# Kernel tuning notes

Hardware: AMD Instinct MI355X
Metric: run time of the kernel (lower is better)

Reference implementation:

```python
import jax, jax.numpy as jnp
import numpy as np


def setup_inputs() -> dict:
    key = jax.random.key(0)
    k1, k2 = jax.random.split(key)
    B, C, H, W = 8, 19, 512, 512
    pred = jax.random.normal(k1, (B, C, H, W), dtype=jnp.float32)
    target = jax.random.randint(k2, (B, H, W), 0, C, dtype=jnp.int64)
    return {"pred": pred, "target": target}


def reference(pred, target):
    # pred: (B, C, H, W) logits; target: (B, H, W) int labels. ignore_index=None.
    C = pred.shape[1]
    probs = jax.nn.softmax(pred, axis=1)
    # flatten pixels: (N, C)
    p = probs.transpose(0, 2, 3, 1).reshape(-1, C)
    t = target.reshape(-1)
    onehot = (t[:, None] == jnp.arange(C)[None, :]).astype(p.dtype)  # (N, C)
    errors = jnp.abs(onehot - p)                                     # (N, C)
    # descending sort of errors per class (batched over the class axis)
    order = jnp.argsort(-errors, axis=0)                             # (N, C)
    errors_sorted = jnp.take_along_axis(errors, order, axis=0)
    target_sorted = jnp.take_along_axis(onehot, order, axis=0)
    gts = target_sorted.sum(axis=0)                                  # (C,)
    intersection = gts[None, :] - jnp.cumsum(target_sorted, axis=0)
    union = gts[None, :] + jnp.cumsum(1.0 - target_sorted, axis=0)
    jaccard = 1.0 - intersection / union                             # (N, C)
    # Lovasz gradient: first-difference along sorted axis, keep first element
    grad = jnp.concatenate([jaccard[:1], jaccard[1:] - jaccard[:-1]], axis=0)
    per_class = jnp.sum(grad * errors_sorted, axis=0)                # (C,)
    present = gts > 0                                                # classes with pixels
    n_present = jnp.maximum(present.sum(), 1).astype(per_class.dtype)
    return jnp.where(present, per_class, 0.0).sum() / n_present
```

## Files before the change

### kernel.cpp

```cpp
#include <hip/hip_runtime.h>
#include <hip/hip_bf16.h>


#define NCLS 19
#define NB 512
#define HWSZ 262144
#define NPIX 2097152
#define HISTW (NCLS * NB)
#define RED_SPLIT 32
#define NBLK 512

__global__ __launch_bounds__(256) void lovasz_hist_kernel(
    const float* __restrict__ pred, const int* __restrict__ tgt,
    unsigned int* __restrict__ gh)
{
    __shared__ unsigned int lh[HISTW];
    for (int j = threadIdx.x; j < HISTW; j += 256) lh[j] = 0u;
    __syncthreads();

    const int stride = gridDim.x * 256;
    for (int g = blockIdx.x * 256 + threadIdx.x; g < (NPIX >> 2); g += stride) {
        const int idx = g << 2;
        const int b  = idx >> 18;
        const int hw = idx & (HWSZ - 1);
        const float* base = pred + ((size_t)b * NCLS) * HWSZ + hw;

        float x0[NCLS], x1[NCLS], x2[NCLS], x3[NCLS];
        #pragma unroll
        for (int c = 0; c < NCLS; ++c) {
            const float4 v = *(const float4*)(base + (size_t)c * HWSZ);
            x0[c] = v.x; x1[c] = v.y; x2[c] = v.z; x3[c] = v.w;
        }
        const int4 t4 = *(const int4*)(tgt + idx);

        float mx0 = x0[0], mx1 = x1[0], mx2 = x2[0], mx3 = x3[0];
        #pragma unroll
        for (int c = 1; c < NCLS; ++c) {
            mx0 = fmaxf(mx0, x0[c]); mx1 = fmaxf(mx1, x1[c]);
            mx2 = fmaxf(mx2, x2[c]); mx3 = fmaxf(mx3, x3[c]);
        }

        float s0 = 0.f, s1 = 0.f, s2 = 0.f, s3 = 0.f;
        #pragma unroll
        for (int c = 0; c < NCLS; ++c) {
            x0[c] = __expf(x0[c] - mx0); s0 += x0[c];
            x1[c] = __expf(x1[c] - mx1); s1 += x1[c];
            x2[c] = __expf(x2[c] - mx2); s2 += x2[c];
            x3[c] = __expf(x3[c] - mx3); s3 += x3[c];
        }
        const float inv0 = 1.f / s0, inv1 = 1.f / s1;
        const float inv2 = 1.f / s2, inv3 = 1.f / s3;

        #pragma unroll
        for (int c = 0; c < NCLS; ++c) {
            {
                const float p = x0[c] * inv0;
                const bool ist = (c == t4.x);
                const float e = ist ? (1.f - p) : p;
                int q = (int)(e * (float)NB);
                q = q < 0 ? 0 : (q > NB - 1 ? NB - 1 : q);
                atomicAdd(&lh[c * NB + q], ist ? 0x10001u : 1u);
            }
            {
                const float p = x1[c] * inv1;
                const bool ist = (c == t4.y);
                const float e = ist ? (1.f - p) : p;
                int q = (int)(e * (float)NB);
                q = q < 0 ? 0 : (q > NB - 1 ? NB - 1 : q);
                atomicAdd(&lh[c * NB + q], ist ? 0x10001u : 1u);
            }
            {
                const float p = x2[c] * inv2;
                const bool ist = (c == t4.z);
                const float e = ist ? (1.f - p) : p;
                int q = (int)(e * (float)NB);
                q = q < 0 ? 0 : (q > NB - 1 ? NB - 1 : q);
                atomicAdd(&lh[c * NB + q], ist ? 0x10001u : 1u);
            }
            {
                const float p = x3[c] * inv3;
                const bool ist = (c == t4.w);
                const float e = ist ? (1.f - p) : p;
                int q = (int)(e * (float)NB);
                q = q < 0 ? 0 : (q > NB - 1 ? NB - 1 : q);
                atomicAdd(&lh[c * NB + q], ist ? 0x10001u : 1u);
            }
        }
    }
    __syncthreads();

    unsigned int* dst = gh + (size_t)blockIdx.x * HISTW;
    for (int j = threadIdx.x; j < HISTW; j += 256) dst[j] = lh[j];
}

__global__ __launch_bounds__(256) void lovasz_reduce_kernel(
    const unsigned int* __restrict__ gh,
    unsigned int* __restrict__ cntp, unsigned int* __restrict__ tcntp, int nblk)
{
    const int j = blockIdx.x * 256 + threadIdx.x;
    const int k = blockIdx.y;
    const int nper = (nblk + RED_SPLIT - 1) / RED_SPLIT;
    const int b0 = k * nper;
    int b1 = b0 + nper; if (b1 > nblk) b1 = nblk;

    unsigned int cs = 0, ts = 0;
    for (int b = b0; b < b1; ++b) {
        const unsigned int w = gh[(size_t)b * HISTW + j];
        cs += w & 0xFFFFu;
        ts += w >> 16;
    }
    cntp[(size_t)k * HISTW + j] = cs;
    tcntp[(size_t)k * HISTW + j] = ts;
}

__global__ __launch_bounds__(512) void lovasz_perclass_kernel(
    const unsigned int* __restrict__ cntp, const unsigned int* __restrict__ tcntp,
    float* __restrict__ pc, int* __restrict__ present)
{
    const int c = blockIdx.x;
    const int d = threadIdx.x;
    const int bin = (NB - 1) - d;
    const int col = c * NB + bin;

    __shared__ unsigned int sI[NB];
    __shared__ unsigned int sK[NB];
    __shared__ float acc;

    unsigned int n = 0, m = 0;
    #pragma unroll
    for (int k = 0; k < RED_SPLIT; ++k) {
        n += cntp[(size_t)k * HISTW + col];
        m += tcntp[(size_t)k * HISTW + col];
    }
    sI[d] = n;
    sK[d] = m;
    if (d == 0) acc = 0.f;
    __syncthreads();

    for (int off = 1; off < NB; off <<= 1) {
        unsigned int vI = 0, vK = 0;
        if (d >= off) { vI = sI[d - off]; vK = sK[d - off]; }
        __syncthreads();
        sI[d] += vI;
        sK[d] += vK;
        __syncthreads();
    }

    const unsigned int I = sI[d];
    const unsigned int K = sK[d];
    const unsigned int G = sK[NB - 1];

    float contrib = 0.f;
    if (n > 0u && G > 0u) {
        const float Jc = 1.f - (float)(G - K) / (float)(G + I - K);
        const unsigned int Ip = I - n, Kp = K - m;
        const float Jp = 1.f - (float)(G - Kp) / (float)(G + Ip - Kp);
        const float v = ((float)bin + 0.5f) * (1.f / (float)NB);
        contrib = v * (Jc - Jp);
    }
    atomicAdd(&acc, contrib);
    __syncthreads();
    if (d == 0) {
        pc[c] = acc;
        present[c] = (G > 0u) ? 1 : 0;
    }
}

__global__ void lovasz_final_kernel(const float* __restrict__ pc,
                                    const int* __restrict__ present,
                                    float* __restrict__ out)
{
    if (blockIdx.x == 0 && threadIdx.x == 0) {
        float s = 0.f;
        int np = 0;
        for (int c = 0; c < NCLS; ++c) {
            if (present[c]) { s += pc[c]; ++np; }
        }
        out[0] = s / (float)(np > 0 ? np : 1);
    }
}

extern "C" void kernel_launch(void* const* d_in, const int* in_sizes, int n_in,
                              void* d_out, int out_size, void* d_ws, size_t ws_size,
                              hipStream_t stream)
{
    const float* pred = (const float*)d_in[0];
    const int* tgt    = (const int*)d_in[1];
    float* out        = (float*)d_out;

    unsigned int* ws = (unsigned int*)d_ws;
    unsigned int* cntp  = ws;
    unsigned int* tcntp = ws + RED_SPLIT * HISTW;
    float* pc           = (float*)(ws + 2 * RED_SPLIT * HISTW);
    int* present        = (int*)(ws + 2 * RED_SPLIT * HISTW + NCLS);
    unsigned int* gh    = ws + 655360;

    const size_t reserved = 655360u * 4u;
    const size_t hbytes = (size_t)HISTW * 4u;
    int nblk = NBLK;
    const size_t avail = (ws_size > reserved) ? (ws_size - reserved) : 0;
    if ((size_t)nblk * hbytes > avail) nblk = (int)(avail / hbytes);
    if (nblk < 32) nblk = 32;

    hipLaunchKernelGGL(lovasz_hist_kernel, dim3(nblk), dim3(256), 0, stream,
                       pred, tgt, gh);
    hipLaunchKernelGGL(lovasz_reduce_kernel, dim3(HISTW / 256, RED_SPLIT), dim3(256), 0, stream,
                       gh, cntp, tcntp, nblk);
    hipLaunchKernelGGL(lovasz_perclass_kernel, dim3(NCLS), dim3(NB), 0, stream,
                       cntp, tcntp, pc, present);
    hipLaunchKernelGGL(lovasz_final_kernel, dim3(1), dim3(64), 0, stream,
                       pc, present, out);
}
```

Measured before the change: 59.50 us.

## Replace per-block histogram dump and reduce kernel with global 64-bit atomics

Each block now merges its shared-memory histogram straight into a zero-initialised global histogram using packed 64-bit atomic adds (count in the low half, target count in the high half). Nonzero bins only are flushed. This removes the per-block histogram writes (about 20 MB), the separate reduce kernel, and the partial-sum reads in the per-class kernel. It adds a memset and global atomic contention across 512 blocks on 9728 addresses.

```diff
diff --git a/kernel.cpp b/kernel.cpp
--- a/kernel.cpp
+++ b/kernel.cpp
@@ -7,12 +7,11 @@
 #define HWSZ 262144
 #define NPIX 2097152
 #define HISTW (NCLS * NB)
-#define RED_SPLIT 32
 #define NBLK 512
 
 __global__ __launch_bounds__(256) void lovasz_hist_kernel(
     const float* __restrict__ pred, const int* __restrict__ tgt,
-    unsigned int* __restrict__ gh)
+    unsigned long long* __restrict__ ghist)
 {
     __shared__ unsigned int lh[HISTW];
     for (int j = threadIdx.x; j < HISTW; j += 256) lh[j] = 0u;
@@ -89,49 +88,32 @@
     }
     __syncthreads();
 
-    unsigned int* dst = gh + (size_t)blockIdx.x * HISTW;
-    for (int j = threadIdx.x; j < HISTW; j += 256) dst[j] = lh[j];
-}
-
-__global__ __launch_bounds__(256) void lovasz_reduce_kernel(
-    const unsigned int* __restrict__ gh,
-    unsigned int* __restrict__ cntp, unsigned int* __restrict__ tcntp, int nblk)
-{
-    const int j = blockIdx.x * 256 + threadIdx.x;
-    const int k = blockIdx.y;
-    const int nper = (nblk + RED_SPLIT - 1) / RED_SPLIT;
-    const int b0 = k * nper;
-    int b1 = b0 + nper; if (b1 > nblk) b1 = nblk;
-
-    unsigned int cs = 0, ts = 0;
-    for (int b = b0; b < b1; ++b) {
-        const unsigned int w = gh[(size_t)b * HISTW + j];
-        cs += w & 0xFFFFu;
-        ts += w >> 16;
+    for (int j = threadIdx.x; j < HISTW; j += 256) {
+        const unsigned int w = lh[j];
+        if (w) {
+            const unsigned long long add =
+                (unsigned long long)(w & 0xFFFFu) |
+                ((unsigned long long)(w >> 16) << 32);
+            atomicAdd(&ghist[j], add);
+        }
     }
-    cntp[(size_t)k * HISTW + j] = cs;
-    tcntp[(size_t)k * HISTW + j] = ts;
 }
 
 __global__ __launch_bounds__(512) void lovasz_perclass_kernel(
-    const unsigned int* __restrict__ cntp, const unsigned int* __restrict__ tcntp,
+    const unsigned long long* __restrict__ ghist,
     float* __restrict__ pc, int* __restrict__ present)
 {
     const int c = blockIdx.x;
     const int d = threadIdx.x;
     const int bin = (NB - 1) - d;
-    const int col = c * NB + bin;
 
     __shared__ unsigned int sI[NB];
     __shared__ unsigned int sK[NB];
     __shared__ float acc;
 
-    unsigned int n = 0, m = 0;
-    #pragma unroll
-    for (int k = 0; k < RED_SPLIT; ++k) {
-        n += cntp[(size_t)k * HISTW + col];
-        m += tcntp[(size_t)k * HISTW + col];
-    }
+    const unsigned long long w = ghist[c * NB + bin];
+    const unsigned int n = (unsigned int)w;
+    const unsigned int m = (unsigned int)(w >> 32);
     sI[d] = n;
     sK[d] = m;
     if (d == 0) acc = 0.f;
@@ -188,26 +170,17 @@
     const int* tgt    = (const int*)d_in[1];
     float* out        = (float*)d_out;
 
-    unsigned int* ws = (unsigned int*)d_ws;
-    unsigned int* cntp  = ws;
-    unsigned int* tcntp = ws + RED_SPLIT * HISTW;
-    float* pc           = (float*)(ws + 2 * RED_SPLIT * HISTW);
-    int* present        = (int*)(ws + 2 * RED_SPLIT * HISTW + NCLS);
-    unsigned int* gh    = ws + 655360;
+    char* wsb = (char*)d_ws;
+    unsigned long long* ghist = (unsigned long long*)wsb;
+    float* pc    = (float*)(wsb + 77824);
+    int* present = (int*)(wsb + 77904);
 
-    const size_t reserved = 655360u * 4u;
-    const size_t hbytes = (size_t)HISTW * 4u;
-    int nblk = NBLK;
-    const size_t avail = (ws_size > reserved) ? (ws_size - reserved) : 0;
-    if ((size_t)nblk * hbytes > avail) nblk = (int)(avail / hbytes);
-    if (nblk < 32) nblk = 32;
+    hipMemsetAsync(ghist, 0, (size_t)HISTW * 8u, stream);
 
-    hipLaunchKernelGGL(lovasz_hist_kernel, dim3(nblk), dim3(256), 0, stream,
-                       pred, tgt, gh);
-    hipLaunchKernelGGL(lovasz_reduce_kernel, dim3(HISTW / 256, RED_SPLIT), dim3(256), 0, stream,
-                       gh, cntp, tcntp, nblk);
+    hipLaunchKernelGGL(lovasz_hist_kernel, dim3(NBLK), dim3(256), 0, stream,
+                       pred, tgt, ghist);
     hipLaunchKernelGGL(lovasz_perclass_kernel, dim3(NCLS), dim3(NB), 0, stream,
-                       cntp, tcntp, pc, present);
+                       ghist, pc, present);
     hipLaunchKernelGGL(lovasz_final_kernel, dim3(1), dim3(64), 0, stream,
                        pc, present, out);
 }
```

Measured after the change: 77.26 us. 1.3x slower.
